# Performance work log

Measured on AMD Instinct MI355X. Metric: run time of the kernel, lower is better.

The kernel has to match this reference:

```python
import jax, jax.numpy as jnp
import numpy as np

TWO_PI = 2.0 * np.pi
OMEGA = 1.0  # frequency scale from init


def setup_inputs() -> dict:
    key = jax.random.key(0)
    ks = jax.random.split(key, 10)
    B, G, D = 2, 32, 3
    C_IN, C, C_OUT, F, L = 4, 128, 2, 128, 4  # in/model/out channels, freqs, n_spectral_convs
    a = jax.random.normal(ks[0], (B, G, G, G, C_IN), dtype=jnp.float32)
    x = jax.random.uniform(ks[1], (B, G, G, G, D), dtype=jnp.float32)
    y = jax.random.uniform(ks[2], (B, G, G, G, D), dtype=jnp.float32)
    fc_in_w = jax.random.normal(ks[3], (C_IN, C), dtype=jnp.float32) / np.sqrt(C_IN)
    fc_in_b = jnp.zeros((C,), dtype=jnp.float32)
    freqs = jax.random.normal(ks[4], (L, F, D), dtype=jnp.float32)  # per-layer spatial frequencies
    w_real = jax.random.normal(ks[5], (L, C, C, F), dtype=jnp.float32) * 0.05
    w_imag = jax.random.normal(ks[6], (L, C, C, F), dtype=jnp.float32) * 0.05
    fc_out_w = jax.random.normal(ks[7], (C, C_OUT), dtype=jnp.float32) / np.sqrt(C)
    fc_out_b = jnp.zeros((C_OUT,), dtype=jnp.float32)
    return {"a": a, "x": x, "y": y, "fc_in_w": fc_in_w, "fc_in_b": fc_in_b,
            "freqs": freqs, "w_real": w_real, "w_imag": w_imag,
            "fc_out_w": fc_out_w, "fc_out_b": fc_out_b}


def _spectral_conv(hf, xin, xout, k, Wc):
    # hf: (B, N, C) real; xin/xout: (B, N, D); k: (F, D); Wc: (C, C, F) complex
    N = hf.shape[1]
    ang_in = TWO_PI * OMEGA * jnp.einsum('bnd,fd->bnf', xin, k)
    phi_in = jnp.exp(-1j * ang_in.astype(jnp.complex64))          # (B, N, F)
    H = jnp.einsum('bnc,bnf->bcf', hf.astype(jnp.complex64), phi_in) / N  # forward transform
    G = jnp.einsum('bcf,cof->bof', H, Wc)                          # per-frequency channel mixing
    ang_out = TWO_PI * OMEGA * jnp.einsum('bnd,fd->bnf', xout, k)
    phi_out = jnp.exp(1j * ang_out.astype(jnp.complex64))          # (B, N, F)
    return jnp.real(jnp.einsum('bof,bnf->bno', G, phi_out))       # inverse evaluation at xout


def reference(a, x, y, fc_in_w, fc_in_b, freqs, w_real, w_imag, fc_out_w, fc_out_b):
    B = a.shape[0]
    spatial = a.shape[1:4]
    hf = jnp.einsum('...i,io->...o', a, fc_in_w) + fc_in_b
    hf = hf.reshape(B, -1, hf.shape[-1])               # (B, N, C)
    xf = x.reshape(B, -1, x.shape[-1])                 # (B, N, D)
    yf = y.reshape(B, -1, y.shape[-1])
    L = freqs.shape[0]
    for l in range(L):
        Wc = (w_real[l] + 1j * w_imag[l]).astype(jnp.complex64)
        pts_out = xf if l < L - 1 else yf              # last conv queries at y
        hf = jax.nn.gelu(_spectral_conv(hf, xf, pts_out, freqs[l], Wc))
    u = jnp.einsum('bnc,co->bno', hf, fc_out_w) + fc_out_b
    return u.reshape(B, *spatial, fc_out_w.shape[-1])
```

## Files before the change

kernel.cpp:

```cpp
#include <hip/hip_runtime.h>
#include <math.h>

#define Bb 2
#define Nn 32768
#define Cc 128
#define Ff 128
#define LL 4
#define SKN 128
#define PS 16448

typedef __attribute__((ext_vector_type(8))) short short8;
typedef __attribute__((ext_vector_type(4))) float float4v;
typedef __attribute__((ext_vector_type(2))) unsigned int uint2v;
typedef unsigned short ushort_t;
typedef unsigned int uint_t;

union frag_cast { short8 s; uint_t u[4]; };
union vec8 { float4v v[2]; float s[8]; };

__device__ inline uint_t asu(float f) { union { float f; uint_t u; } x; x.f = f; return x.u; }
__device__ inline float asf(uint_t u) { union { uint_t u; float f; } x; x.u = u; return x.f; }
__device__ inline uint_t pack_hi(float v0, float v1) {
    return __builtin_amdgcn_perm(asu(v1), asu(v0), 0x07060302u);
}
__device__ inline float resid(float v) { return v - asf(asu(v) & 0xffff0000u); }

typedef __attribute__((address_space(1))) const uint_t guint;
typedef __attribute__((address_space(3))) uint_t luint;
__device__ inline void gload16(const uint_t* g, uint_t* l) {
    __builtin_amdgcn_global_load_lds((guint*)g, (luint*)l, 16, 0, 0);
}

#define LBAR() asm volatile("s_waitcnt lgkmcnt(0)\n\ts_barrier" ::: "memory")

__global__ __launch_bounds__(256) void prep_xt(const float* __restrict__ x,
                                               const float* __restrict__ y,
                                               float* __restrict__ xT,
                                               float* __restrict__ yT) {
    int i = blockIdx.x * 256 + threadIdx.x;
    int b = i >> 15, n = i & 32767;
    const float* xp = x + (size_t)i * 3;
    const float* yp = y + (size_t)i * 3;
    size_t base = ((size_t)(b * 3) << 15) + n;
    xT[base] = xp[0]; xT[base + (1 << 15)] = xp[1]; xT[base + (2 << 15)] = xp[2];
    yT[base] = yp[0]; yT[base + (1 << 15)] = yp[1]; yT[base + (2 << 15)] = yp[2];
}

__global__ __launch_bounds__(256) void in_proj(const float* __restrict__ a,
                                               const float* __restrict__ w,
                                               const float* __restrict__ bias,
                                               uint_t* __restrict__ hfTh,
                                               uint_t* __restrict__ hfTl) {
    int idx = blockIdx.x * 256 + threadIdx.x;
    int np = idx & 16383;
    int c = (idx >> 14) & 127;
    int b = idx >> 21;
    int n = np * 2;
    const float* ap = a + (((size_t)(b << 15)) + n) * 4;
    float s0 = bias[c], s1 = s0;
#pragma unroll
    for (int i = 0; i < 4; ++i) { s0 += ap[i] * w[i * Cc + c]; s1 += ap[4 + i] * w[i * Cc + c]; }
    hfTh[idx] = pack_hi(s0, s1);
    hfTl[idx] = pack_hi(resid(s0), resid(s1));
}

__global__ __launch_bounds__(256) void fwd_lds(const uint_t* __restrict__ hfTh,
                                               const uint_t* __restrict__ hfTl,
                                               const float* __restrict__ xT,
                                               const float* __restrict__ freqs,
                                               float* __restrict__ Spart) {
    __shared__ __align__(16) uint_t Ah_s[2][1024], Al_s[2][1024];

    const int sk = blockIdx.x;
    const int ct = blockIdx.y & 1, ft = blockIdx.y >> 1;
    const int b = blockIdx.z;
    const int tid = threadIdx.x, lane = tid & 63, wave = tid >> 6;
    const int h = wave & 1, wn = wave >> 1;
    const int fr = lane & 15, kg = lane >> 4;
    const int crow0 = b * 128 + ct * 64;

    float kx[2], ky[2], kz[2];
#pragma unroll
    for (int ni = 0; ni < 2; ++ni) {
        int f = ft * 64 + wn * 32 + ni * 16 + fr;
        kx[ni] = freqs[f * 3 + 0];
        ky[ni] = freqs[f * 3 + 1];
        kz[ni] = freqs[f * 3 + 2];
    }

    const float* xb = xT + ((size_t)(b * 3) << 15);

    const int srow = wave * 16 + (lane >> 2);
    const size_t gbase = ((size_t)(crow0 + srow) << 14) + (size_t)((lane & 3) * 4);
    const int npair0 = sk * 128;

    float4v acc[4][2];
#pragma unroll
    for (int mi = 0; mi < 4; ++mi)
#pragma unroll
        for (int ni = 0; ni < 2; ++ni) acc[mi][ni] = (float4v){0.f, 0.f, 0.f, 0.f};

    vec8 X0[2], X1[2], X2[2];
    gload16(hfTh + gbase + npair0, &Ah_s[0][wave * 256]);
    gload16(hfTl + gbase + npair0, &Al_s[0][wave * 256]);
    {
        const int nbase = sk * 256 + kg * 8;
        X0[0].v[0] = *(const float4v*)(xb + nbase);
        X0[0].v[1] = *(const float4v*)(xb + nbase + 4);
        X1[0].v[0] = *(const float4v*)(xb + (1 << 15) + nbase);
        X1[0].v[1] = *(const float4v*)(xb + (1 << 15) + nbase + 4);
        X2[0].v[0] = *(const float4v*)(xb + (2 << 15) + nbase);
        X2[0].v[1] = *(const float4v*)(xb + (2 << 15) + nbase + 4);
    }

#pragma unroll
    for (int kt = 0; kt < 8; ++kt) {
        const int cur = kt & 1, nxt = cur ^ 1;
        __syncthreads();
        if (kt < 7) {
            gload16(hfTh + gbase + npair0 + (kt + 1) * 16, &Ah_s[nxt][wave * 256]);
            gload16(hfTl + gbase + npair0 + (kt + 1) * 16, &Al_s[nxt][wave * 256]);
            const int nbase2 = sk * 256 + (kt + 1) * 32 + kg * 8;
            X0[nxt].v[0] = *(const float4v*)(xb + nbase2);
            X0[nxt].v[1] = *(const float4v*)(xb + nbase2 + 4);
            X1[nxt].v[0] = *(const float4v*)(xb + (1 << 15) + nbase2);
            X1[nxt].v[1] = *(const float4v*)(xb + (1 << 15) + nbase2 + 4);
            X2[nxt].v[0] = *(const float4v*)(xb + (2 << 15) + nbase2);
            X2[nxt].v[1] = *(const float4v*)(xb + (2 << 15) + nbase2 + 4);
        }
        float r[16], tv[16];
#pragma unroll
        for (int ni = 0; ni < 2; ++ni)
#pragma unroll
            for (int q = 0; q < 4; ++q) {
                float rv0 = X0[cur].s[2 * q] * kx[ni] + X1[cur].s[2 * q] * ky[ni] + X2[cur].s[2 * q] * kz[ni];
                float rv1 = X0[cur].s[2 * q + 1] * kx[ni] + X1[cur].s[2 * q + 1] * ky[ni] + X2[cur].s[2 * q + 1] * kz[ni];
                r[ni * 8 + 2 * q] = __builtin_amdgcn_fractf(rv0);
                r[ni * 8 + 2 * q + 1] = __builtin_amdgcn_fractf(rv1);
            }
        if (h) {
#pragma unroll
            for (int i = 0; i < 16; ++i) tv[i] = __builtin_amdgcn_sinf(r[i]);
        } else {
#pragma unroll
            for (int i = 0; i < 16; ++i) tv[i] = __builtin_amdgcn_cosf(r[i]);
        }
        frag_cast bhf[2], blf[2];
#pragma unroll
        for (int ni = 0; ni < 2; ++ni)
#pragma unroll
            for (int q = 0; q < 4; ++q) {
                float v0 = tv[ni * 8 + 2 * q], v1 = tv[ni * 8 + 2 * q + 1];
                bhf[ni].u[q] = pack_hi(v0, v1);
                blf[ni].u[q] = pack_hi(resid(v0), resid(v1));
            }
#pragma unroll
        for (int mi = 0; mi < 4; ++mi) {
            frag_cast ah, al;
            ah.s = *(const short8*)&Ah_s[cur][(mi * 16 + fr) * 16 + kg * 4];
            al.s = *(const short8*)&Al_s[cur][(mi * 16 + fr) * 16 + kg * 4];
#pragma unroll
            for (int ni = 0; ni < 2; ++ni) {
                acc[mi][ni] = __builtin_amdgcn_mfma_f32_16x16x32_bf16(ah.s, bhf[ni].s, acc[mi][ni], 0, 0, 0);
                acc[mi][ni] = __builtin_amdgcn_mfma_f32_16x16x32_bf16(ah.s, blf[ni].s, acc[mi][ni], 0, 0, 0);
                acc[mi][ni] = __builtin_amdgcn_mfma_f32_16x16x32_bf16(al.s, bhf[ni].s, acc[mi][ni], 0, 0, 0);
            }
        }
    }

    float* op = Spart + (size_t)((b * 2 + h) * SKN + sk) * PS;
#pragma unroll
    for (int mi = 0; mi < 4; ++mi)
#pragma unroll
        for (int ni = 0; ni < 2; ++ni)
#pragma unroll
            for (int r2 = 0; r2 < 4; ++r2) {
                int c = ct * 64 + mi * 16 + kg * 4 + r2;
                int f = ft * 64 + wn * 32 + ni * 16 + fr;
                op[c * 128 + f] = acc[mi][ni][r2];
            }
}

__global__ __launch_bounds__(256) void reduce_kernel(const float* __restrict__ Spart,
                                                     float* __restrict__ S) {
    __shared__ float red[4][64];
    const int chunk = blockIdx.x, bh = blockIdx.y;
    const int tid = threadIdx.x;
    const int cfl = tid & 63, q = tid >> 6;
    const float* p = Spart + (size_t)bh * SKN * PS + (size_t)(q * 32) * PS + chunk * 64 + cfl;
    float s = 0.0f;
#pragma unroll 8
    for (int k = 0; k < 32; ++k) s += p[(size_t)k * PS];
    red[q][cfl] = s;
    __syncthreads();
    if (tid < 64) {
        float t = red[0][tid] + red[1][tid] + red[2][tid] + red[3][tid];
        S[bh * 16384 + chunk * 64 + tid] = t;
    }
}

__global__ __launch_bounds__(256) void mix_kernel(const float* __restrict__ S,
                                                  const float* __restrict__ Wre,
                                                  const float* __restrict__ Wim,
                                                  uint_t* __restrict__ Gh,
                                                  uint_t* __restrict__ Gl) {
    __shared__ float Stile[4][128][16];
    const int ot = blockIdx.x;
    const int ft = blockIdx.y;
    const int tid = threadIdx.x;
    const int fl = tid & 15, ol = (tid >> 4) & 1, cg = tid >> 5;
    const int o = ot * 2 + ol, f0 = ft * 16;

    for (int i = tid; i < 8192; i += 256) {
        int bh = i >> 11, c = (i >> 4) & 127, ff = i & 15;
        Stile[bh][c][ff] = S[(size_t)bh * 16384 + c * 128 + f0 + ff];
    }
    __syncthreads();

    float g0 = 0.f, g1 = 0.f, g2 = 0.f, g3 = 0.f;
#pragma unroll 4
    for (int c = cg * 16; c < cg * 16 + 16; ++c) {
        float wr = Wre[((size_t)(c * 128 + o)) * 128 + f0 + fl];
        float wi = Wim[((size_t)(c * 128 + o)) * 128 + f0 + fl];
        float sc0 = Stile[0][c][fl], ss0 = Stile[1][c][fl];
        float sc1 = Stile[2][c][fl], ss1 = Stile[3][c][fl];
        g0 += sc0 * wr + ss0 * wi;  g1 += ss0 * wr - sc0 * wi;
        g2 += sc1 * wr + ss1 * wi;  g3 += ss1 * wr - sc1 * wi;
    }
    __syncthreads();
    float4v* rp = (float4v*)Stile;
    rp[cg * 32 + ol * 16 + fl] = (float4v){g0, g1, g2, g3};
    __syncthreads();
    if (tid < 32) {
        int tol = tid >> 4, tfl = tid & 15;
        float4v r = rp[tid];
#pragma unroll
        for (int j = 1; j < 8; ++j) r += rp[j * 32 + tid];
        const float invN = 1.0f / (float)Nn;
        float gre0 = r[0] * invN, gmi0 = r[1] * invN;
        float gre1 = r[2] * invN, gmi1 = r[3] * invN;
        int oo = ot * 2 + tol;
        Gh[(0 * 128 + oo) * 128 + f0 + tfl] = pack_hi(gre0, gmi0);
        Gl[(0 * 128 + oo) * 128 + f0 + tfl] = pack_hi(resid(gre0), resid(gmi0));
        Gh[(1 * 128 + oo) * 128 + f0 + tfl] = pack_hi(gre1, gmi1);
        Gl[(1 * 128 + oo) * 128 + f0 + tfl] = pack_hi(resid(gre1), resid(gmi1));
    }
}

__global__ __launch_bounds__(256, 2) void inv_reg(const uint_t* __restrict__ Gh,
                                                  const uint_t* __restrict__ Gl,
                                                  const float* __restrict__ ptsT,
                                                  const float* __restrict__ freqs,
                                                  uint_t* __restrict__ hfTh,
                                                  uint_t* __restrict__ hfTl) {
    __shared__ __align__(16) float kxs[128], kys[128], kzs[128];
    __shared__ __align__(16) uint_t Ah_s[4096];
    __shared__ __align__(16) uint_t Al_s[4096];
    const int nt = blockIdx.x, b = blockIdx.y;
    const int tid = threadIdx.x, lane = tid & 63, wn = tid >> 6;
    const int fr = lane & 15, kg = lane >> 4;

    if (tid < 128) {
        kxs[tid] = freqs[tid * 3 + 0];
        kys[tid] = freqs[tid * 3 + 1];
        kzs[tid] = freqs[tid * 3 + 2];
    }

    frag_cast bh[8][2], bl[8][2];
#pragma unroll
    for (int kt = 0; kt < 8; ++kt)
#pragma unroll
        for (int ni = 0; ni < 2; ++ni) {
            size_t gi = ((size_t)(b * 128 + wn * 32 + ni * 16 + fr)) * 128 + kt * 16 + kg * 4;
            bh[kt][ni].s = *(const short8*)(Gh + gi);
            bl[kt][ni].s = *(const short8*)(Gl + gi);
        }

    const float* pb = ptsT + ((size_t)(b * 3) << 15);
    const int stripe0 = nt * 64;

    float px[2][2], py[2][2], pz[2][2];
#pragma unroll
    for (int it = 0; it < 2; ++it)
#pragma unroll
        for (int mi = 0; mi < 2; ++mi) {
            int n = stripe0 + it * 32 + mi * 16 + fr;
            px[it][mi] = pb[n]; py[it][mi] = pb[(1 << 15) + n]; pz[it][mi] = pb[(2 << 15) + n];
        }

    __syncthreads();

#pragma unroll
    for (int it = 0; it < 2; ++it) {
        const int n0 = stripe0 + it * 32;

#pragma unroll
        for (int kk = 0; kk < 2; ++kk) {
            const int kt = wn * 2 + kk;
            float4v kxv = *(const float4v*)&kxs[kt * 16 + kg * 4];
            float4v kyv = *(const float4v*)&kys[kt * 16 + kg * 4];
            float4v kzv = *(const float4v*)&kzs[kt * 16 + kg * 4];
#pragma unroll
            for (int mi = 0; mi < 2; ++mi) {
                frag_cast ah, al;
#pragma unroll
                for (int q = 0; q < 4; ++q) {
                    float rev = px[it][mi] * kxv[q] + py[it][mi] * kyv[q] + pz[it][mi] * kzv[q];
                    float rr = __builtin_amdgcn_fractf(rev);
                    float cv = __builtin_amdgcn_cosf(rr);
                    float sv = __builtin_amdgcn_sinf(rr);
                    ah.u[q] = pack_hi(cv, sv);
                    al.u[q] = pack_hi(resid(cv), resid(sv));
                }
                *(short8*)&Ah_s[((mi * 8 + kt) * 64 + lane) * 4] = ah.s;
                *(short8*)&Al_s[((mi * 8 + kt) * 64 + lane) * 4] = al.s;
            }
        }
        LBAR();

        float4v acc[2][2];
#pragma unroll
        for (int mi = 0; mi < 2; ++mi)
#pragma unroll
            for (int ni = 0; ni < 2; ++ni) acc[mi][ni] = (float4v){0.f, 0.f, 0.f, 0.f};

#pragma unroll
        for (int kt = 0; kt < 8; ++kt) {
#pragma unroll
            for (int mi = 0; mi < 2; ++mi) {
                frag_cast ah, al;
                ah.s = *(const short8*)&Ah_s[((mi * 8 + kt) * 64 + lane) * 4];
                al.s = *(const short8*)&Al_s[((mi * 8 + kt) * 64 + lane) * 4];
#pragma unroll
                for (int ni = 0; ni < 2; ++ni) {
                    acc[mi][ni] = __builtin_amdgcn_mfma_f32_16x16x32_bf16(ah.s, bh[kt][ni].s, acc[mi][ni], 0, 0, 0);
                    acc[mi][ni] = __builtin_amdgcn_mfma_f32_16x16x32_bf16(ah.s, bl[kt][ni].s, acc[mi][ni], 0, 0, 0);
                    acc[mi][ni] = __builtin_amdgcn_mfma_f32_16x16x32_bf16(al.s, bh[kt][ni].s, acc[mi][ni], 0, 0, 0);
                }
            }
        }
        LBAR();

#pragma unroll
        for (int mi = 0; mi < 2; ++mi)
#pragma unroll
            for (int ni = 0; ni < 2; ++ni) {
                float g[4];
#pragma unroll
                for (int r2 = 0; r2 < 4; ++r2) {
                    float v = acc[mi][ni][r2];
                    float u2 = 1.5957691216057308f * (v + 0.044715f * v * v * v);
                    float t = 1.0f - 2.0f / (1.0f + __expf(u2));
                    g[r2] = 0.5f * v * (1.0f + t);
                }
                int o = wn * 32 + ni * 16 + fr;
                int nb = n0 + mi * 16 + kg * 4;
                size_t di = ((size_t)(b * 128 + o) << 14) + (nb >> 1);
                uint2v hv = { pack_hi(g[0], g[1]), pack_hi(g[2], g[3]) };
                uint2v lv = { pack_hi(resid(g[0]), resid(g[1])), pack_hi(resid(g[2]), resid(g[3])) };
                *(uint2v*)(hfTh + di) = hv;
                *(uint2v*)(hfTl + di) = lv;
            }
    }
}

__global__ __launch_bounds__(256) void out_proj(const uint_t* __restrict__ hfTh,
                                                const uint_t* __restrict__ hfTl,
                                                const float* __restrict__ w,
                                                const float* __restrict__ bias,
                                                float* __restrict__ u) {
    int i = blockIdx.x * 256 + threadIdx.x;
    int b = i >> 14, np = i & 16383;
    const uint_t* hp = hfTh + ((size_t)(b * 128) << 14) + np;
    const uint_t* lp = hfTl + ((size_t)(b * 128) << 14) + np;
    float s0a = bias[0], s1a = bias[1], s0b = bias[0], s1b = bias[1];
#pragma unroll 4
    for (int c = 0; c < 128; ++c) {
        uint_t hv = hp[(size_t)c << 14], lv = lp[(size_t)c << 14];
        float v0 = asf(hv << 16) + asf(lv << 16);
        float v1 = asf(hv & 0xffff0000u) + asf(lv & 0xffff0000u);
        float w0 = w[c * 2 + 0], w1 = w[c * 2 + 1];
        s0a += v0 * w0; s1a += v0 * w1;
        s0b += v1 * w0; s1b += v1 * w1;
    }
    float4v o4 = {s0a, s1a, s0b, s1b};
    *(float4v*)(u + ((size_t)(b << 15) + np * 2) * 2) = o4;
}

extern "C" void kernel_launch(void* const* d_in, const int* in_sizes, int n_in,
                              void* d_out, int out_size, void* d_ws, size_t ws_size,
                              hipStream_t stream) {
    const float* a        = (const float*)d_in[0];
    const float* x        = (const float*)d_in[1];
    const float* y        = (const float*)d_in[2];
    const float* fc_in_w  = (const float*)d_in[3];
    const float* fc_in_b  = (const float*)d_in[4];
    const float* freqs    = (const float*)d_in[5];
    const float* w_real   = (const float*)d_in[6];
    const float* w_imag   = (const float*)d_in[7];
    const float* fc_out_w = (const float*)d_in[8];
    const float* fc_out_b = (const float*)d_in[9];
    float* out = (float*)d_out;

    uint_t* ws    = (uint_t*)d_ws;
    uint_t* hfTh  = ws;
    uint_t* hfTl  = hfTh + (size_t)Bb * Cc * Nn / 2;
    float*  Spart = (float*)(hfTl + (size_t)Bb * Cc * Nn / 2);
    float*  S     = Spart + (size_t)Bb * 2 * SKN * PS;
    uint_t* Gh    = (uint_t*)(S + (size_t)Bb * 2 * Cc * Ff);
    uint_t* Gl    = Gh + (size_t)Bb * Cc * Ff;
    float*  xT    = (float*)(Gl + (size_t)Bb * Cc * Ff);
    float*  yT    = xT + (size_t)Bb * 3 * Nn;

    prep_xt<<<(Bb * Nn) / 256, 256, 0, stream>>>(x, y, xT, yT);
    in_proj<<<(Bb * Cc * Nn / 2) / 256, 256, 0, stream>>>(a, fc_in_w, fc_in_b, hfTh, hfTl);

    for (int l = 0; l < LL; ++l) {
        const float* k   = freqs  + (size_t)l * Ff * 3;
        const float* Wre = w_real + (size_t)l * Cc * Cc * Ff;
        const float* Wim = w_imag + (size_t)l * Cc * Cc * Ff;
        const float* pT  = (l < LL - 1) ? xT : yT;

        fwd_lds<<<dim3(SKN, 4, Bb), 256, 0, stream>>>(hfTh, hfTl, xT, k, Spart);
        reduce_kernel<<<dim3(256, 4), 256, 0, stream>>>(Spart, S);
        mix_kernel<<<dim3(64, 8), 256, 0, stream>>>(S, Wre, Wim, Gh, Gl);
        inv_reg<<<dim3(512, Bb), 256, 0, stream>>>(Gh, Gl, pT, k, hfTh, hfTl);
    }

    out_proj<<<(Bb * Nn / 2) / 256, 256, 0, stream>>>(hfTh, hfTl, fc_out_w, fc_out_b, out);
}
```

Measured before the change: 388.4 us.

## Widen forward-transform blocks to cover all channels and fuse output projection into last inverse

The forward-transform kernel now uses 512-thread blocks, each covering all 128 channels and all 128 frequencies. Before, four blocks per K-slice each recomputed their own sin/cos phase tiles, so this cuts redundant trig work and duplicate loads of the x coordinates. The last layer's inverse kernel is templated so it applies the output projection in-register: a shuffle and LDS reduction over channels writes `u` directly. That removes the separate `out_proj` pass and the last write and re-read of the hidden state. The cost is fewer, larger forward blocks with more accumulator registers, which may lower latency hiding.

Result: faster. 367.5 us (-5.4%).

```diff
diff --git a/kernel.cpp b/kernel.cpp
--- a/kernel.cpp
+++ b/kernel.cpp
@@ -64,25 +64,23 @@
     hfTl[idx] = pack_hi(resid(s0), resid(s1));
 }
 
-__global__ __launch_bounds__(256) void fwd_lds(const uint_t* __restrict__ hfTh,
-                                               const uint_t* __restrict__ hfTl,
-                                               const float* __restrict__ xT,
-                                               const float* __restrict__ freqs,
-                                               float* __restrict__ Spart) {
-    __shared__ __align__(16) uint_t Ah_s[2][1024], Al_s[2][1024];
+__global__ __launch_bounds__(512, 2) void fwd_lds(const uint_t* __restrict__ hfTh,
+                                                  const uint_t* __restrict__ hfTl,
+                                                  const float* __restrict__ xT,
+                                                  const float* __restrict__ freqs,
+                                                  float* __restrict__ Spart) {
+    __shared__ __align__(16) uint_t Ah_s[2][2048], Al_s[2][2048];
 
     const int sk = blockIdx.x;
-    const int ct = blockIdx.y & 1, ft = blockIdx.y >> 1;
-    const int b = blockIdx.z;
+    const int b = blockIdx.y;
     const int tid = threadIdx.x, lane = tid & 63, wave = tid >> 6;
     const int h = wave & 1, wn = wave >> 1;
     const int fr = lane & 15, kg = lane >> 4;
-    const int crow0 = b * 128 + ct * 64;
 
     float kx[2], ky[2], kz[2];
 #pragma unroll
     for (int ni = 0; ni < 2; ++ni) {
-        int f = ft * 64 + wn * 32 + ni * 16 + fr;
+        int f = wn * 32 + ni * 16 + fr;
         kx[ni] = freqs[f * 3 + 0];
         ky[ni] = freqs[f * 3 + 1];
         kz[ni] = freqs[f * 3 + 2];
@@ -91,12 +89,12 @@
     const float* xb = xT + ((size_t)(b * 3) << 15);
 
     const int srow = wave * 16 + (lane >> 2);
-    const size_t gbase = ((size_t)(crow0 + srow) << 14) + (size_t)((lane & 3) * 4);
+    const size_t gbase = ((size_t)(b * 128 + srow) << 14) + (size_t)((lane & 3) * 4);
     const int npair0 = sk * 128;
 
-    float4v acc[4][2];
-#pragma unroll
-    for (int mi = 0; mi < 4; ++mi)
+    float4v acc[8][2];
+#pragma unroll
+    for (int mi = 0; mi < 8; ++mi)
 #pragma unroll
         for (int ni = 0; ni < 2; ++ni) acc[mi][ni] = (float4v){0.f, 0.f, 0.f, 0.f};
 
@@ -155,7 +153,7 @@
                 blf[ni].u[q] = pack_hi(resid(v0), resid(v1));
             }
 #pragma unroll
-        for (int mi = 0; mi < 4; ++mi) {
+        for (int mi = 0; mi < 8; ++mi) {
             frag_cast ah, al;
             ah.s = *(const short8*)&Ah_s[cur][(mi * 16 + fr) * 16 + kg * 4];
             al.s = *(const short8*)&Al_s[cur][(mi * 16 + fr) * 16 + kg * 4];
@@ -170,13 +168,13 @@
 
     float* op = Spart + (size_t)((b * 2 + h) * SKN + sk) * PS;
 #pragma unroll
-    for (int mi = 0; mi < 4; ++mi)
+    for (int mi = 0; mi < 8; ++mi)
 #pragma unroll
         for (int ni = 0; ni < 2; ++ni)
 #pragma unroll
             for (int r2 = 0; r2 < 4; ++r2) {
-                int c = ct * 64 + mi * 16 + kg * 4 + r2;
-                int f = ft * 64 + wn * 32 + ni * 16 + fr;
+                int c = mi * 16 + kg * 4 + r2;
+                int f = wn * 32 + ni * 16 + fr;
                 op[c * 128 + f] = acc[mi][ni][r2];
             }
 }
@@ -247,15 +245,20 @@
     }
 }
 
+template <int LAST>
 __global__ __launch_bounds__(256, 2) void inv_reg(const uint_t* __restrict__ Gh,
                                                   const uint_t* __restrict__ Gl,
                                                   const float* __restrict__ ptsT,
                                                   const float* __restrict__ freqs,
                                                   uint_t* __restrict__ hfTh,
-                                                  uint_t* __restrict__ hfTl) {
+                                                  uint_t* __restrict__ hfTl,
+                                                  const float* __restrict__ ow,
+                                                  const float* __restrict__ ob,
+                                                  float* __restrict__ u) {
     __shared__ __align__(16) float kxs[128], kys[128], kzs[128];
     __shared__ __align__(16) uint_t Ah_s[4096];
     __shared__ __align__(16) uint_t Al_s[4096];
+    __shared__ float redo[4][32][2];
     const int nt = blockIdx.x, b = blockIdx.y;
     const int tid = threadIdx.x, lane = tid & 63, wn = tid >> 6;
     const int fr = lane & 15, kg = lane >> 4;
@@ -275,6 +278,16 @@
             bh[kt][ni].s = *(const short8*)(Gh + gi);
             bl[kt][ni].s = *(const short8*)(Gl + gi);
         }
+
+    float w0v[2], w1v[2];
+    if (LAST) {
+#pragma unroll
+        for (int ni = 0; ni < 2; ++ni) {
+            int o = wn * 32 + ni * 16 + fr;
+            w0v[ni] = ow[o * 2 + 0];
+            w1v[ni] = ow[o * 2 + 1];
+        }
+    }
 
     const float* pb = ptsT + ((size_t)(b * 3) << 15);
     const int stripe0 = nt * 64;
@@ -341,6 +354,15 @@
         }
         LBAR();
 
+        float ps[2][2][4];
+        if (LAST) {
+#pragma unroll
+            for (int mi = 0; mi < 2; ++mi)
+#pragma unroll
+                for (int j = 0; j < 2; ++j)
+#pragma unroll
+                    for (int r2 = 0; r2 < 4; ++r2) ps[mi][j][r2] = 0.f;
+        }
 #pragma unroll
         for (int mi = 0; mi < 2; ++mi)
 #pragma unroll
@@ -353,38 +375,54 @@
                     float t = 1.0f - 2.0f / (1.0f + __expf(u2));
                     g[r2] = 0.5f * v * (1.0f + t);
                 }
-                int o = wn * 32 + ni * 16 + fr;
-                int nb = n0 + mi * 16 + kg * 4;
-                size_t di = ((size_t)(b * 128 + o) << 14) + (nb >> 1);
-                uint2v hv = { pack_hi(g[0], g[1]), pack_hi(g[2], g[3]) };
-                uint2v lv = { pack_hi(resid(g[0]), resid(g[1])), pack_hi(resid(g[2]), resid(g[3])) };
-                *(uint2v*)(hfTh + di) = hv;
-                *(uint2v*)(hfTl + di) = lv;
-            }
-    }
-}
-
-__global__ __launch_bounds__(256) void out_proj(const uint_t* __restrict__ hfTh,
-                                                const uint_t* __restrict__ hfTl,
-                                                const float* __restrict__ w,
-                                                const float* __restrict__ bias,
-                                                float* __restrict__ u) {
-    int i = blockIdx.x * 256 + threadIdx.x;
-    int b = i >> 14, np = i & 16383;
-    const uint_t* hp = hfTh + ((size_t)(b * 128) << 14) + np;
-    const uint_t* lp = hfTl + ((size_t)(b * 128) << 14) + np;
-    float s0a = bias[0], s1a = bias[1], s0b = bias[0], s1b = bias[1];
-#pragma unroll 4
-    for (int c = 0; c < 128; ++c) {
-        uint_t hv = hp[(size_t)c << 14], lv = lp[(size_t)c << 14];
-        float v0 = asf(hv << 16) + asf(lv << 16);
-        float v1 = asf(hv & 0xffff0000u) + asf(lv & 0xffff0000u);
-        float w0 = w[c * 2 + 0], w1 = w[c * 2 + 1];
-        s0a += v0 * w0; s1a += v0 * w1;
-        s0b += v1 * w0; s1b += v1 * w1;
-    }
-    float4v o4 = {s0a, s1a, s0b, s1b};
-    *(float4v*)(u + ((size_t)(b << 15) + np * 2) * 2) = o4;
+                if (!LAST) {
+                    int o = wn * 32 + ni * 16 + fr;
+                    int nb = n0 + mi * 16 + kg * 4;
+                    size_t di = ((size_t)(b * 128 + o) << 14) + (nb >> 1);
+                    uint2v hv = { pack_hi(g[0], g[1]), pack_hi(g[2], g[3]) };
+                    uint2v lv = { pack_hi(resid(g[0]), resid(g[1])), pack_hi(resid(g[2]), resid(g[3])) };
+                    *(uint2v*)(hfTh + di) = hv;
+                    *(uint2v*)(hfTl + di) = lv;
+                } else {
+#pragma unroll
+                    for (int r2 = 0; r2 < 4; ++r2) {
+                        ps[mi][0][r2] += g[r2] * w0v[ni];
+                        ps[mi][1][r2] += g[r2] * w1v[ni];
+                    }
+                }
+            }
+
+        if (LAST) {
+#pragma unroll
+            for (int mi = 0; mi < 2; ++mi)
+#pragma unroll
+                for (int j = 0; j < 2; ++j)
+#pragma unroll
+                    for (int r2 = 0; r2 < 4; ++r2) {
+                        float v = ps[mi][j][r2];
+                        v += __shfl_xor(v, 1);
+                        v += __shfl_xor(v, 2);
+                        v += __shfl_xor(v, 4);
+                        v += __shfl_xor(v, 8);
+                        ps[mi][j][r2] = v;
+                    }
+            if (fr == 0) {
+#pragma unroll
+                for (int mi = 0; mi < 2; ++mi)
+#pragma unroll
+                    for (int r2 = 0; r2 < 4; ++r2) {
+                        redo[wn][mi * 16 + kg * 4 + r2][0] = ps[mi][0][r2];
+                        redo[wn][mi * 16 + kg * 4 + r2][1] = ps[mi][1][r2];
+                    }
+            }
+            LBAR();
+            if (tid < 64) {
+                int nl = tid >> 1, j = tid & 1;
+                float val = ob[j] + redo[0][nl][j] + redo[1][nl][j] + redo[2][nl][j] + redo[3][nl][j];
+                u[((size_t)((b << 15) + n0 + nl)) * 2 + j] = val;
+            }
+        }
+    }
 }
 
 extern "C" void kernel_launch(void* const* d_in, const int* in_sizes, int n_in,
@@ -421,11 +459,15 @@
         const float* Wim = w_imag + (size_t)l * Cc * Cc * Ff;
         const float* pT  = (l < LL - 1) ? xT : yT;
 
-        fwd_lds<<<dim3(SKN, 4, Bb), 256, 0, stream>>>(hfTh, hfTl, xT, k, Spart);
+        fwd_lds<<<dim3(SKN, Bb), 512, 0, stream>>>(hfTh, hfTl, xT, k, Spart);
         reduce_kernel<<<dim3(256, 4), 256, 0, stream>>>(Spart, S);
         mix_kernel<<<dim3(64, 8), 256, 0, stream>>>(S, Wre, Wim, Gh, Gl);
-        inv_reg<<<dim3(512, Bb), 256, 0, stream>>>(Gh, Gl, pT, k, hfTh, hfTl);
-    }
-
-    out_proj<<<(Bb * Nn / 2) / 256, 256, 0, stream>>>(hfTh, hfTl, fc_out_w, fc_out_b, out);
-}
+        if (l < LL - 1) {
+            inv_reg<0><<<dim3(512, Bb), 256, 0, stream>>>(Gh, Gl, pT, k, hfTh, hfTl,
+                                                          nullptr, nullptr, nullptr);
+        } else {
+            inv_reg<1><<<dim3(512, Bb), 256, 0, stream>>>(Gh, Gl, pT, k, hfTh, hfTl,
+                                                          fc_out_w, fc_out_b, out);
+        }
+    }
+}
```
